# Kernel optimization log

Hardware: AMD Instinct MI355X
Metric: run time of the kernel (lower is better)

## Reference

```python
import jax, jax.numpy as jnp
import numpy as np

POI, EMB, UNITS, QDIM, B = 5000, 256, 512, 256, 64


def setup_inputs() -> dict:
    key = jax.random.key(0)
    ks = jax.random.split(key, 16)
    s = 0.05
    return {
        "x": jax.random.randint(ks[0], (B,), 0, POI),
        "query": jax.random.normal(ks[1], (B, QDIM), jnp.float32),
        "poi_embedding": jax.random.normal(ks[2], (POI, EMB), jnp.float32),
        "A_hat": jax.random.normal(ks[3], (B, B), jnp.float32),
        "dec_hidden": jax.random.normal(ks[4], (B, UNITS), jnp.float32),
        "cat_dec_hidden": jax.random.normal(ks[5], (1, B, UNITS), jnp.float32),
        # GRUCell params (keras order z, r, h; reset_after=True -> bias [2, 3*units])
        "gru_kernel": jax.random.normal(ks[6], (EMB + QDIM, 3 * UNITS), jnp.float32) * s,
        "gru_rec_kernel": jax.random.normal(ks[7], (UNITS, 3 * UNITS), jnp.float32) * s,
        "gru_bias": jax.random.normal(ks[8], (2, 3 * UNITS), jnp.float32) * s,
        # Bahdanau attention params
        "W1_w": jax.random.normal(ks[9], (EMB, UNITS), jnp.float32) * s,
        "W1_b": jnp.zeros((UNITS,), jnp.float32),
        "W2_w": jax.random.normal(ks[10], (UNITS, UNITS), jnp.float32) * s,
        "W2_b": jnp.zeros((UNITS,), jnp.float32),
        "V_w": jax.random.normal(ks[11], (UNITS, 1), jnp.float32) * s,
        "V_b": jnp.zeros((1,), jnp.float32),
        # output dense: concat(context EMB, output_ UNITS, cat_hidden UNITS) -> POI
        "fc_w": jax.random.normal(ks[12], (EMB + 2 * UNITS, POI), jnp.float32) * s,
        "fc_b": jnp.zeros((POI,), jnp.float32),
    }


def _gru_cell(x, h, kernel, rec_kernel, bias):
    # keras GRUCell, reset_after=True, gate order (z, r, h)
    xm = x @ kernel + bias[0]        # [B, 3U]
    hm = h @ rec_kernel + bias[1]    # [B, 3U]
    xz, xr, xh = jnp.split(xm, 3, axis=-1)
    hz, hr, hh = jnp.split(hm, 3, axis=-1)
    z = jax.nn.sigmoid(xz + hz)
    r = jax.nn.sigmoid(xr + hr)
    h_cand = jnp.tanh(xh + r * hh)
    h_new = z * h + (1.0 - z) * h_cand
    return h_new, h_new


def reference(x, query, poi_embedding, A_hat, dec_hidden, cat_dec_hidden,
              gru_kernel, gru_rec_kernel, gru_bias,
              W1_w, W1_b, W2_w, W2_b, V_w, V_b, fc_w, fc_b):
    emb = poi_embedding
    x1 = jnp.concatenate([emb[x], query], axis=1)          # [B, EMB+QDIM]
    output_, state = _gru_cell(x1, dec_hidden, gru_kernel, gru_rec_kernel, gru_bias)
    # Bahdanau attention: values are the full embedding table [POI, EMB]
    v_proj = emb @ W1_w + W1_b                              # [POI, U]
    q_proj = output_ @ W2_w + W2_b                          # [B, U]
    score = jnp.tanh(v_proj[None, :, :] + q_proj[:, None, :]) @ V_w + V_b  # [B, POI, 1]
    attn = jax.nn.softmax(score, axis=1)                    # [B, POI, 1]
    context = jnp.sum(attn * emb[None, :, :], axis=1)       # [B, EMB]
    out_cat = jnp.concatenate([context, output_, cat_dec_hidden[0]], axis=1)
    logits = out_cat @ fc_w + fc_b                          # [B, POI]
    return (logits, state, output_)
```

## Files before the change

### kernel.cpp

```cpp
#include <hip/hip_runtime.h>
#include <hip/hip_bf16.h>

typedef __bf16 bf16;
typedef __bf16 bf16x8 __attribute__((ext_vector_type(8)));
typedef float f32x4 __attribute__((ext_vector_type(4)));

#define BB 64
#define EMB 256
#define UNITS 512
#define POI 5000
#define KCAT 1280
#define SCLD 5024
#define L2E 1.4426950408889634f

__device__ __forceinline__ float rcp_(float x){ return __builtin_amdgcn_rcpf(x); }
__device__ __forceinline__ float exp2_(float x){ return __builtin_amdgcn_exp2f(x); }

__device__ __forceinline__ f32x4 mm16f(const float* __restrict__ A, const float* __restrict__ B,
                                       int lda, int ldb, int K, int mr, int nc, int lane){
  int q = lane >> 4;
  f32x4 acc = {0.f,0.f,0.f,0.f};
  const float* ap = A + (size_t)mr*lda + q*8;
  const float* bp = B + (size_t)(q*8)*ldb + nc;
#pragma unroll 2
  for(int k0 = 0; k0 < K; k0 += 32){
    f32x4 a0 = *(const f32x4*)ap;
    f32x4 a1 = *(const f32x4*)(ap+4);
    bf16x8 a, b;
#pragma unroll
    for(int j=0;j<4;j++){ a[j] = (bf16)a0[j]; a[4+j] = (bf16)a1[j]; }
#pragma unroll
    for(int j=0;j<8;j++) b[j] = (bf16)bp[(size_t)j*ldb];
    acc = __builtin_amdgcn_mfma_f32_16x16x32_bf16(a, b, acc, 0, 0, 0);
    ap += 32; bp += (size_t)32*ldb;
  }
  return acc;
}

__global__ __launch_bounds__(256) void k_gru(const int* __restrict__ x,
    const float* __restrict__ query, const float* __restrict__ emb, const float* __restrict__ h0,
    const float* __restrict__ gruK, const float* __restrict__ gruR,
    float* __restrict__ xmP, float* __restrict__ hmP){
  int lane = threadIdx.x & 63, w = threadIdx.x >> 6;
  int col = blockIdx.x*16 + (lane & 15);
  int m = w*16 + (lane & 15);
  int z = blockIdx.z;
  const float* A; const float* B; int lda, mr;
  if(blockIdx.y == 0){
    B = gruK + (size_t)(z*256)*1536;
    if(z == 0){ A = emb;   mr = x[m]; lda = EMB; }
    else      { A = query; mr = m;    lda = 256; }
  } else {
    B = gruR + (size_t)(z*256)*1536;
    A = h0 + z*256; mr = m; lda = UNITS;
  }
  f32x4 acc = mm16f(A, B, lda, 1536, 256, mr, col, lane);
  float* C = (blockIdx.y ? hmP : xmP) + (size_t)z*BB*1536;
  int rb = w*16 + (lane >> 4)*4;
#pragma unroll
  for(int r=0;r<4;r++) C[(size_t)(rb+r)*1536 + col] = acc[r];
}

__global__ void k_gates(const float* __restrict__ xmP, const float* __restrict__ hmP,
                        const float* __restrict__ bias, const float* __restrict__ h0,
                        const float* __restrict__ catd,
                        float* __restrict__ hn, float* __restrict__ outc, float* __restrict__ dout){
  int b = blockIdx.x, u = threadIdx.x;
  const float* x0 = xmP + b*1536; const float* x1s = xmP + (size_t)BB*1536 + b*1536;
  const float* h0s = hmP + b*1536; const float* h1s = hmP + (size_t)BB*1536 + b*1536;
  float xz = x0[u]      + x1s[u]      + bias[u];
  float xg = x0[512+u]  + x1s[512+u]  + bias[512+u];
  float xh = x0[1024+u] + x1s[1024+u] + bias[1024+u];
  float hz = h0s[u]      + h1s[u]      + bias[1536+u];
  float hg = h0s[512+u]  + h1s[512+u]  + bias[2048+u];
  float hh = h0s[1024+u] + h1s[1024+u] + bias[2560+u];
  float z = rcp_(1.f + exp2_(-L2E*(xz+hz)));
  float r = rcp_(1.f + exp2_(-L2E*(xg+hg)));
  float ca = xh + r*hh;
  ca = fminf(fmaxf(ca, -15.f), 15.f);
  float e = exp2_(2.f*L2E*ca);
  float hc = (e - 1.f)*rcp_(e + 1.f);
  float h = h0[b*512+u];
  float v = z*h + (1.f - z)*hc;
  hn[b*512+u] = v;
  outc[b*KCAT + 256 + u] = v;
  outc[b*KCAT + 768 + u] = catd[(size_t)b*512 + u];
  dout[(size_t)POI*BB + (size_t)b*512 + u] = v;
  dout[(size_t)POI*BB + (size_t)BB*512 + (size_t)b*512 + u] = v;
}

__global__ __launch_bounds__(256) void k_qproj(const float* __restrict__ hn, const float* __restrict__ W2,
                        const float* __restrict__ W2b, float* __restrict__ Eq){
  int lane = threadIdx.x & 63, w = threadIdx.x >> 6;
  int col = blockIdx.x*16 + (lane & 15);
  f32x4 acc = mm16f(hn, W2, UNITS, UNITS, UNITS, w*16 + (lane & 15), col, lane);
  float bn = W2b[col];
  int rb = w*16 + (lane >> 4)*4;
#pragma unroll
  for(int r=0;r<4;r++){
    float v = (acc[r] + bn)*(2.f*L2E);
    Eq[(rb+r)*UNITS + col] = exp2_(fminf(fmaxf(v, -28.f), 28.f));
  }
}

__global__ __launch_bounds__(256) void k_vscore(const float* __restrict__ emb, const float* __restrict__ W1,
    const float* __restrict__ W1b, const float* __restrict__ Eq,
    const float* __restrict__ Vw, float* __restrict__ sc){
  __shared__ float evs[16][68];
  __shared__ float Qs[64][68];
  __shared__ float vws[64];
  int t = threadIdx.x, lane = t & 63, w = t >> 6;
  int p0 = blockIdx.x*16, uh = blockIdx.y*64;
  int mr = p0 + (lane & 15); if(mr > POI-1) mr = POI-1;
  {
    int ncl = w*16 + (lane & 15);
    f32x4 acc = mm16f(emb, W1, EMB, UNITS, EMB, mr, uh + ncl, lane);
    float bn = W1b[uh + ncl];
    int rb = (lane >> 4)*4;
#pragma unroll
    for(int r=0;r<4;r++){
      float v = (acc[r] + bn)*(2.f*L2E);
      evs[rb+r][ncl] = exp2_(fminf(fmaxf(v, -28.f), 28.f));
    }
  }
  for(int i=t;i<1024;i+=256){ int b=i>>4, u4=i&15; *(f32x4*)&Qs[b][u4*4] = *(const f32x4*)&Eq[b*UNITS + uh + u4*4]; }
  if(t < 64) vws[t] = Vw[uh + t];
  __syncthreads();
  int tp = t & 7, tb = t >> 3;
  float s00=0.f, s01=0.f, s10=0.f, s11=0.f;
#pragma unroll
  for(int u4=0;u4<16;u4++){
    f32x4 e0 = *(f32x4*)&evs[2*tp][u4*4];
    f32x4 e1 = *(f32x4*)&evs[2*tp+1][u4*4];
    f32x4 q0 = *(f32x4*)&Qs[2*tb][u4*4];
    f32x4 q1 = *(f32x4*)&Qs[2*tb+1][u4*4];
    f32x4 w4 = *(f32x4*)&vws[u4*4];
#pragma unroll
    for(int h=0;h<2;h++){
      int i0 = 2*h, i1 = 2*h+1;
      float w0 = w4[i0], w1 = w4[i1];
      float da, db;
      da = __builtin_fmaf(e0[i0], q0[i0], 1.f); db = __builtin_fmaf(e0[i1], q0[i1], 1.f);
      s00 = __builtin_fmaf(__builtin_fmaf(w0, db, w1*da), rcp_(da*db), s00);
      da = __builtin_fmaf(e0[i0], q1[i0], 1.f); db = __builtin_fmaf(e0[i1], q1[i1], 1.f);
      s01 = __builtin_fmaf(__builtin_fmaf(w0, db, w1*da), rcp_(da*db), s01);
      da = __builtin_fmaf(e1[i0], q0[i0], 1.f); db = __builtin_fmaf(e1[i1], q0[i1], 1.f);
      s10 = __builtin_fmaf(__builtin_fmaf(w0, db, w1*da), rcp_(da*db), s10);
      da = __builtin_fmaf(e1[i0], q1[i0], 1.f); db = __builtin_fmaf(e1[i1], q1[i1], 1.f);
      s11 = __builtin_fmaf(__builtin_fmaf(w0, db, w1*da), rcp_(da*db), s11);
    }
  }
  int pA = p0 + 2*tp, bA = 2*tb;
  if(pA < POI){
    atomicAdd(&sc[(size_t)bA*SCLD + pA],     s00);
    atomicAdd(&sc[(size_t)(bA+1)*SCLD + pA], s01);
  }
  if(pA+1 < POI){
    atomicAdd(&sc[(size_t)bA*SCLD + pA+1],     s10);
    atomicAdd(&sc[(size_t)(bA+1)*SCLD + pA+1], s11);
  }
}

__global__ __launch_bounds__(1024) void k_softmax(float* __restrict__ sc, float* __restrict__ outc){
  __shared__ float red[1024];
  int b = blockIdx.x, t = threadIdx.x;
  if(t < 256) outc[b*KCAT + t] = 0.f;
  float* sA = sc + (size_t)b*SCLD;
  float sum = 0.f;
  for(int p=t;p<POI;p+=1024){
    float wv = exp2_(-2.f*L2E*sA[p]);
    sA[p] = wv;
    sum += wv;
  }
  red[t] = sum; __syncthreads();
  for(int o=512;o>0;o>>=1){ if(t<o) red[t]+=red[t+o]; __syncthreads(); }
  float iv = rcp_(red[0]);
  for(int p=t;p<POI;p+=1024) sA[p] *= iv;
  if(t < SCLD-POI) sA[POI + t] = 0.f;
}

__global__ __launch_bounds__(256) void k_ctx(const float* __restrict__ wb, const float* __restrict__ emb,
                                             float* __restrict__ outc){
  int lane = threadIdx.x & 63, w = threadIdx.x >> 6;
  int n = blockIdx.x*16 + (lane & 15);
  int ky = blockIdx.y;
  int kbeg = ky*384;
  int mr = w*16 + (lane & 15);
  f32x4 acc = mm16f(wb + kbeg, emb + (size_t)kbeg*EMB, SCLD, EMB, 384, mr, n, lane);
  if(ky == 12){
    int q = lane >> 4;
    const float* ap = wb + (size_t)mr*SCLD + 4992 + q*8;
    bf16x8 a, bfr;
#pragma unroll
    for(int j=0;j<8;j++) a[j] = (bf16)ap[j];
#pragma unroll
    for(int j=0;j<8;j++){
      int k = 4992 + q*8 + j; int kc = k < POI ? k : POI-1;
      bfr[j] = (bf16)emb[(size_t)kc*EMB + n];
    }
    acc = __builtin_amdgcn_mfma_f32_16x16x32_bf16(a, bfr, acc, 0, 0, 0);
  }
  int rb = w*16 + (lane >> 4)*4;
#pragma unroll
  for(int r=0;r<4;r++) atomicAdd(&outc[(size_t)(rb+r)*KCAT + n], acc[r]);
}

__global__ __launch_bounds__(256) void k_logits(const float* __restrict__ A, const float* __restrict__ Bw,
                        const float* __restrict__ fcb, float* __restrict__ out){
  int lane = threadIdx.x & 63, w = threadIdx.x >> 6;
  int n = blockIdx.x*16 + (lane & 15);
  int nc = n < POI ? n : POI-1;
  int ky = blockIdx.y, kbeg = ky*320;
  f32x4 acc = mm16f(A + kbeg, Bw + (size_t)kbeg*POI, KCAT, POI, 320,
                    w*16 + (lane & 15), nc, lane);
  int rb = w*16 + (lane >> 4)*4;
  if(n < POI){
    float bn = (ky == 0) ? fcb[n] : 0.f;
#pragma unroll
    for(int r=0;r<4;r++) atomicAdd(&out[(size_t)(rb+r)*POI + n], acc[r] + bn);
  }
}

extern "C" void kernel_launch(void* const* d_in, const int* in_sizes, int n_in,
                              void* d_out, int out_size, void* d_ws, size_t ws_size,
                              hipStream_t stream){
  const int*   x     = (const int*)d_in[0];
  const float* query = (const float*)d_in[1];
  const float* emb   = (const float*)d_in[2];
  const float* h0    = (const float*)d_in[4];
  const float* catd  = (const float*)d_in[5];
  const float* gruK  = (const float*)d_in[6];
  const float* gruR  = (const float*)d_in[7];
  const float* gruB  = (const float*)d_in[8];
  const float* W1    = (const float*)d_in[9];
  const float* W1b   = (const float*)d_in[10];
  const float* W2    = (const float*)d_in[11];
  const float* W2b   = (const float*)d_in[12];
  const float* Vw    = (const float*)d_in[13];
  const float* fcw   = (const float*)d_in[15];
  const float* fcb   = (const float*)d_in[16];
  float* out = (float*)d_out;

  char* ws = (char*)d_ws;
  size_t off = 0;
  auto alloc = [&](size_t bytes)->void*{ void* p = ws + off; off += (bytes + 255) & ~(size_t)255; return p; };
  float* outc = (float*)alloc((size_t)BB*KCAT*4);
  float* xmP  = (float*)alloc((size_t)2*BB*1536*4);
  float* hmP  = (float*)alloc((size_t)2*BB*1536*4);
  float* hn   = (float*)alloc((size_t)BB*512*4);
  float* Eq   = (float*)alloc((size_t)BB*512*4);
  float* sc   = (float*)alloc((size_t)BB*SCLD*4);

  hipMemsetAsync(out, 0, (size_t)BB*POI*4, stream);
  hipMemsetAsync(sc, 0, (size_t)BB*SCLD*4, stream);
  k_gru    <<<dim3(96,2,2), 256, 0, stream>>>(x, query, emb, h0, gruK, gruR, xmP, hmP);
  k_gates  <<<BB, 512, 0, stream>>>(xmP, hmP, gruB, h0, catd, hn, outc, out);
  k_qproj  <<<32, 256, 0, stream>>>(hn, W2, W2b, Eq);
  k_vscore <<<dim3(313,8), 256, 0, stream>>>(emb, W1, W1b, Eq, Vw, sc);
  k_softmax<<<BB, 1024, 0, stream>>>(sc, outc);
  k_ctx    <<<dim3(16,13), 256, 0, stream>>>(sc, emb, outc);
  k_logits <<<dim3(313,4), 256, 0, stream>>>(outc, fcw, fcb, out);
}
```

Measured before the change: 229.2 us.

## Replace score atomics with per-split partial buffers and drop memsets

The attention-score kernel now writes each unit-split's partial sums to its own buffer slice instead of atomically adding into one zeroed buffer, and the softmax kernel sums the eight slices. This removes both hipMemsetAsync calls; the output zeroing moves into the gates kernel. The q-projection kernel is relaunched as 128 single-wave blocks, and the score inner loop is simplified to one reciprocal per element instead of a paired-reciprocal trick. The trade-off is extra partial-buffer traffic in softmax and twice as many reciprocals in the score loop.

```diff
diff --git a/kernel.cpp b/kernel.cpp
--- a/kernel.cpp
+++ b/kernel.cpp
@@ -11,6 +11,7 @@
 #define POI 5000
 #define KCAT 1280
 #define SCLD 5024
+#define NSPL 8
 #define L2E 1.4426950408889634f
 
 __device__ __forceinline__ float rcp_(float x){ return __builtin_amdgcn_rcpf(x); }
@@ -66,6 +67,7 @@
                         const float* __restrict__ catd,
                         float* __restrict__ hn, float* __restrict__ outc, float* __restrict__ dout){
   int b = blockIdx.x, u = threadIdx.x;
+  for(int p=u;p<POI;p+=512) dout[(size_t)b*POI + p] = 0.f;
   const float* x0 = xmP + b*1536; const float* x1s = xmP + (size_t)BB*1536 + b*1536;
   const float* h0s = hmP + b*1536; const float* h1s = hmP + (size_t)BB*1536 + b*1536;
   float xz = x0[u]      + x1s[u]      + bias[u];
@@ -89,13 +91,14 @@
   dout[(size_t)POI*BB + (size_t)BB*512 + (size_t)b*512 + u] = v;
 }
 
-__global__ __launch_bounds__(256) void k_qproj(const float* __restrict__ hn, const float* __restrict__ W2,
+__global__ __launch_bounds__(64) void k_qproj(const float* __restrict__ hn, const float* __restrict__ W2,
                         const float* __restrict__ W2b, float* __restrict__ Eq){
-  int lane = threadIdx.x & 63, w = threadIdx.x >> 6;
-  int col = blockIdx.x*16 + (lane & 15);
-  f32x4 acc = mm16f(hn, W2, UNITS, UNITS, UNITS, w*16 + (lane & 15), col, lane);
+  int lane = threadIdx.x;
+  int m0 = (blockIdx.x & 3)*16;
+  int col = (blockIdx.x >> 2)*16 + (lane & 15);
+  f32x4 acc = mm16f(hn, W2, UNITS, UNITS, UNITS, m0 + (lane & 15), col, lane);
   float bn = W2b[col];
-  int rb = w*16 + (lane >> 4)*4;
+  int rb = m0 + (lane >> 4)*4;
 #pragma unroll
   for(int r=0;r<4;r++){
     float v = (acc[r] + bn)*(2.f*L2E);
@@ -105,7 +108,7 @@
 
 __global__ __launch_bounds__(256) void k_vscore(const float* __restrict__ emb, const float* __restrict__ W1,
     const float* __restrict__ W1b, const float* __restrict__ Eq,
-    const float* __restrict__ Vw, float* __restrict__ sc){
+    const float* __restrict__ Vw, float* __restrict__ scS){
   __shared__ float evs[16][68];
   __shared__ float Qs[64][68];
   __shared__ float vws[64];
@@ -123,7 +126,7 @@
       evs[rb+r][ncl] = exp2_(fminf(fmaxf(v, -28.f), 28.f));
     }
   }
-  for(int i=t;i<1024;i+=256){ int b=i>>4, u4=i&15; *(f32x4*)&Qs[b][u4*4] = *(const f32x4*)&Eq[b*UNITS + uh + u4*4]; }
+  for(int i=t;i<4096;i+=256){ int b=i>>6, u=i&63; Qs[b][u] = Eq[b*UNITS + uh + u]; }
   if(t < 64) vws[t] = Vw[uh + t];
   __syncthreads();
   int tp = t & 7, tb = t >> 3;
@@ -136,29 +139,18 @@
     f32x4 q1 = *(f32x4*)&Qs[2*tb+1][u4*4];
     f32x4 w4 = *(f32x4*)&vws[u4*4];
 #pragma unroll
-    for(int h=0;h<2;h++){
-      int i0 = 2*h, i1 = 2*h+1;
-      float w0 = w4[i0], w1 = w4[i1];
-      float da, db;
-      da = __builtin_fmaf(e0[i0], q0[i0], 1.f); db = __builtin_fmaf(e0[i1], q0[i1], 1.f);
-      s00 = __builtin_fmaf(__builtin_fmaf(w0, db, w1*da), rcp_(da*db), s00);
-      da = __builtin_fmaf(e0[i0], q1[i0], 1.f); db = __builtin_fmaf(e0[i1], q1[i1], 1.f);
-      s01 = __builtin_fmaf(__builtin_fmaf(w0, db, w1*da), rcp_(da*db), s01);
-      da = __builtin_fmaf(e1[i0], q0[i0], 1.f); db = __builtin_fmaf(e1[i1], q0[i1], 1.f);
-      s10 = __builtin_fmaf(__builtin_fmaf(w0, db, w1*da), rcp_(da*db), s10);
-      da = __builtin_fmaf(e1[i0], q1[i0], 1.f); db = __builtin_fmaf(e1[i1], q1[i1], 1.f);
-      s11 = __builtin_fmaf(__builtin_fmaf(w0, db, w1*da), rcp_(da*db), s11);
+    for(int e=0;e<4;e++){
+      float wv = w4[e];
+      s00 += wv * rcp_(e0[e]*q0[e] + 1.f);
+      s01 += wv * rcp_(e0[e]*q1[e] + 1.f);
+      s10 += wv * rcp_(e1[e]*q0[e] + 1.f);
+      s11 += wv * rcp_(e1[e]*q1[e] + 1.f);
     }
   }
+  float* s = scS + (size_t)blockIdx.y*BB*SCLD;
   int pA = p0 + 2*tp, bA = 2*tb;
-  if(pA < POI){
-    atomicAdd(&sc[(size_t)bA*SCLD + pA],     s00);
-    atomicAdd(&sc[(size_t)(bA+1)*SCLD + pA], s01);
-  }
-  if(pA+1 < POI){
-    atomicAdd(&sc[(size_t)bA*SCLD + pA+1],     s10);
-    atomicAdd(&sc[(size_t)(bA+1)*SCLD + pA+1], s11);
-  }
+  if(pA < POI)  { s[(size_t)bA*SCLD + pA]   = s00; s[(size_t)(bA+1)*SCLD + pA]   = s01; }
+  if(pA+1 < POI){ s[(size_t)bA*SCLD + pA+1] = s10; s[(size_t)(bA+1)*SCLD + pA+1] = s11; }
 }
 
 __global__ __launch_bounds__(1024) void k_softmax(float* __restrict__ sc, float* __restrict__ outc){
@@ -168,7 +160,10 @@
   float* sA = sc + (size_t)b*SCLD;
   float sum = 0.f;
   for(int p=t;p<POI;p+=1024){
-    float wv = exp2_(-2.f*L2E*sA[p]);
+    float a = sA[p];
+#pragma unroll
+    for(int y=1;y<NSPL;y++) a += sA[(size_t)y*BB*SCLD + p];
+    float wv = exp2_(-2.f*L2E*a);
     sA[p] = wv;
     sum += wv;
   }
@@ -249,14 +244,12 @@
   float* hmP  = (float*)alloc((size_t)2*BB*1536*4);
   float* hn   = (float*)alloc((size_t)BB*512*4);
   float* Eq   = (float*)alloc((size_t)BB*512*4);
-  float* sc   = (float*)alloc((size_t)BB*SCLD*4);
-
-  hipMemsetAsync(out, 0, (size_t)BB*POI*4, stream);
-  hipMemsetAsync(sc, 0, (size_t)BB*SCLD*4, stream);
+  float* sc   = (float*)alloc((size_t)NSPL*BB*SCLD*4);
+
   k_gru    <<<dim3(96,2,2), 256, 0, stream>>>(x, query, emb, h0, gruK, gruR, xmP, hmP);
   k_gates  <<<BB, 512, 0, stream>>>(xmP, hmP, gruB, h0, catd, hn, outc, out);
-  k_qproj  <<<32, 256, 0, stream>>>(hn, W2, W2b, Eq);
-  k_vscore <<<dim3(313,8), 256, 0, stream>>>(emb, W1, W1b, Eq, Vw, sc);
+  k_qproj  <<<128, 64, 0, stream>>>(hn, W2, W2b, Eq);
+  k_vscore <<<dim3(313,NSPL), 256, 0, stream>>>(emb, W1, W1b, Eq, Vw, sc);
   k_softmax<<<BB, 1024, 0, stream>>>(sc, outc);
   k_ctx    <<<dim3(16,13), 256, 0, stream>>>(sc, emb, outc);
   k_logits <<<dim3(313,4), 256, 0, stream>>>(outc, fcw, fcb, out);
```

Measured after the change: 238.2 us. 3.9% more time.
